# Performance work log

Hardware: AMD Instinct MI355X
Metric: run time of the kernel (lower is better)

Reference implementation:

```python
import jax, jax.numpy as jnp
import numpy as np

H = W = 512
K = 16          # max instance id (ids 1..K; 0 = background)
N_SIGMA = 1
FG_W = 1.0
W_INST, W_VAR, W_SEED = 1.0, 10.0, 1.0


def _xym(h, w, dtype):
    # torch: linspace(0,1,512) grids, sliced to [:, :h, :w]
    x = jnp.linspace(0.0, 1.0, 512)[:w]
    y = jnp.linspace(0.0, 1.0, 512)[:h]
    xm = jnp.broadcast_to(x[None, :], (h, w))
    ym = jnp.broadcast_to(y[:, None], (h, w))
    return jnp.stack([xm, ym], 0).astype(dtype)  # [2,h,w]


def _lovasz_hinge(logits, labels):
    # logits, labels: flat [P]; labels in {0,1} float
    signs = 2.0 * labels - 1.0
    errors = 1.0 - logits * signs
    perm = jnp.argsort(-errors)           # descending sort
    errors_sorted = errors[perm]
    gt_sorted = labels[perm]
    gts = gt_sorted.sum()
    inter = gts - jnp.cumsum(gt_sorted)
    union = gts + jnp.cumsum(1.0 - gt_sorted)
    jac = 1.0 - inter / union
    grad = jnp.concatenate([jac[:1], jac[1:] - jac[:-1]])
    # lovasz grad is computed from .data (detached) in the torch impl
    return jnp.dot(jax.nn.relu(errors_sorted), jax.lax.stop_gradient(grad))


def _per_instance(mask, spatial_emb, sigma, seed, xym):
    # mask: [H,W] float {0,1}; spatial_emb: [2,H,W]; sigma: [n_sigma,H,W]; seed: [H,W]
    cnt = mask.sum()
    safe = jnp.maximum(cnt, 1.0)
    center = jnp.sum(xym * mask, (1, 2)) / safe                        # [2] (to_center=True)
    s = jnp.sum(sigma * mask, (1, 2)) / safe                           # [n_sigma]
    var = jnp.sum((sigma - jax.lax.stop_gradient(s)[:, None, None]) ** 2 * mask) / (N_SIGMA * safe)
    s_exp = jnp.exp(s * 10.0)
    dist = jnp.exp(-jnp.sum((spatial_emb - center[:, None, None]) ** 2 * s_exp[:, None, None], 0))  # [H,W]
    inst = _lovasz_hinge(dist.ravel() * 2.0 - 1.0, mask.ravel())
    seed_l = FG_W * jnp.sum((seed - jax.lax.stop_gradient(dist)) ** 2 * mask)
    present = cnt > 0
    z = jnp.zeros((), dist.dtype)
    return (jnp.where(present, var, z), jnp.where(present, inst, z),
            jnp.where(present, seed_l, z), present.astype(dist.dtype))


def _per_image(pred, inst, lab, xym):
    spatial_emb = jnp.tanh(pred[0:2]) + xym                            # [2,H,W]
    sigma = pred[2:2 + N_SIGMA]                                        # [n_sigma,H,W]
    seed = jax.nn.sigmoid(pred[2 + N_SIGMA])                           # [H,W]
    ids = jnp.arange(1, K + 1)
    masks = (inst[None] == ids[:, None, None]).astype(pred.dtype)      # [K,H,W]
    var, instl, seedl, pres = jax.vmap(
        _per_instance, in_axes=(0, None, None, None, None))(masks, spatial_emb, sigma, seed, xym)
    obj = pres.sum()
    safe_obj = jnp.maximum(obj, 1.0)
    bg = (lab == 0).astype(pred.dtype)
    seed_total = (jnp.sum(seed ** 2 * bg) + seedl.sum()) / float(H * W)
    return W_INST * instl.sum() / safe_obj + W_VAR * var.sum() / safe_obj + W_SEED * seed_total


def setup_inputs() -> dict:
    key = jax.random.key(0)
    k1, k2, k3 = jax.random.split(key, 3)
    prediction = jax.random.normal(k1, (8, 4, H, W), dtype=jnp.float32)
    instances = jax.random.randint(k2, (8, H, W), 0, K + 1, dtype=jnp.int32)
    labels = jax.random.randint(k3, (8, H, W), 0, 2, dtype=jnp.int32)
    return {"prediction": prediction, "instances": instances, "labels": labels}


def reference(prediction, instances, labels):
    xym = _xym(prediction.shape[2], prediction.shape[3], prediction.dtype)
    losses = jax.vmap(_per_image, in_axes=(0, 0, 0, None))(prediction, instances, labels, xym)
    return losses.mean() + prediction.sum() * 0.0
```

## Files before the change

kernel.cpp:

```cpp
#include <hip/hip_runtime.h>

#define HH 512
#define WW 512
#define NPIX (HH*WW)
#define KK 16
#define BB 8
#define NB 128
#define NBP 136
#define CHS 128
#define CHV 128

__device__ __forceinline__ float fast_rcp(float x){ return __builtin_amdgcn_rcpf(x); }
__device__ __forceinline__ float fast_tanh(float x){
  x = fminf(fmaxf(x, -15.f), 15.f);
  float t = __expf(2.f*x);
  return (t-1.f)*fast_rcp(t+1.f);
}
__device__ __forceinline__ float fast_sigmoid(float x){
  x = fminf(fmaxf(x, -30.f), 30.f);
  return fast_rcp(1.f+__expf(-x));
}

__device__ __forceinline__ float dpp_row_sum16(float v){
  v += __int_as_float(__builtin_amdgcn_update_dpp(0, __float_as_int(v), 0x111, 0xf, 0xf, true));
  v += __int_as_float(__builtin_amdgcn_update_dpp(0, __float_as_int(v), 0x112, 0xf, 0xf, true));
  v += __int_as_float(__builtin_amdgcn_update_dpp(0, __float_as_int(v), 0x114, 0xf, 0xf, true));
  v += __int_as_float(__builtin_amdgcn_update_dpp(0, __float_as_int(v), 0x118, 0xf, 0xf, true));
  return v;
}

__global__ void __launch_bounds__(256) k_sums(
    const float* __restrict__ pred, const int* __restrict__ inst,
    const int* __restrict__ lab, float* __restrict__ partial_s ,
    float* __restrict__ partial_b ) {
  const int bid = blockIdx.x;
  const int b  = bid & 7;
  const int ch = bid >> 3;
  const int tid = threadIdx.x;
  const int wave = tid >> 6, lane = tid & 63;
  __shared__ float lred[KK][16][5];
  __shared__ float lbg[4];
  const float inv = 1.f/511.f;
  const float* ps = pred + (size_t)b*4*NPIX + 2*NPIX;
  const float* pd = ps + NPIX;
  const int*   ib = inst + (size_t)b*NPIX;
  const int*   lb = lab  + (size_t)b*NPIX;
  const int p = ch*2048 + tid*8;
  int4   iv0 = *(const int4*)(ib + p),     iv1 = *(const int4*)(ib + p + 4);
  int4   lv0 = *(const int4*)(lb + p),     lv1 = *(const int4*)(lb + p + 4);
  float4 sv0 = *(const float4*)(ps + p),   sv1 = *(const float4*)(ps + p + 4);
  float4 dv0 = *(const float4*)(pd + p),   dv1 = *(const float4*)(pd + p + 4);
  const float ym  = (float)(p >> 9) * inv;
  const float xm0 = (float)(p & (WW-1)) * inv;
  int   ida[8] = {iv0.x, iv0.y, iv0.z, iv0.w, iv1.x, iv1.y, iv1.z, iv1.w};
  int   laa[8] = {lv0.x, lv0.y, lv0.z, lv0.w, lv1.x, lv1.y, lv1.z, lv1.w};
  float sga[8] = {sv0.x, sv0.y, sv0.z, sv0.w, sv1.x, sv1.y, sv1.z, sv1.w};
  float sda[8] = {dv0.x, dv0.y, dv0.z, dv0.w, dv1.x, dv1.y, dv1.z, dv1.w};
  float xja[8], sg2[8];
  #pragma unroll
  for (int j = 0; j < 8; ++j) {
    xja[j] = xm0 + (float)j*inv;
    sg2[j] = sga[j]*sga[j];
  }

  float sbg = 0.f;
  #pragma unroll
  for (int j = 0; j < 8; ++j)
    if (laa[j] == 0) { float sd = fast_sigmoid(sda[j]); sbg += sd*sd; }
  #pragma unroll
  for (int off = 32; off; off >>= 1) sbg += __shfl_down(sbg, off);
  if (lane == 0) lbg[wave] = sbg;

  #pragma unroll
  for (int k = 0; k < KK; ++k) {
    float c = 0.f, sx = 0.f, ss = 0.f, sq = 0.f;
    #pragma unroll
    for (int j = 0; j < 8; ++j) {
      float m = (ida[j] == k+1) ? 1.f : 0.f;
      c  += m;
      sx = fmaf(m, xja[j], sx);
      ss = fmaf(m, sga[j], ss);
      sq = fmaf(m, sg2[j], sq);
    }
    c  = dpp_row_sum16(c);
    sx = dpp_row_sum16(sx);
    ss = dpp_row_sum16(ss);
    sq = dpp_row_sum16(sq);
    if ((lane & 15) == 15) {
      int g = wave*4 + (lane >> 4);
      lred[k][g][0] = c;  lred[k][g][1] = sx; lred[k][g][2] = c*ym;
      lred[k][g][3] = ss; lred[k][g][4] = sq;
    }
  }
  __syncthreads();
  if (tid < KK) {
    #pragma unroll
    for (int comp = 0; comp < 5; ++comp) {
      float a = 0.f;
      #pragma unroll
      for (int g = 0; g < 16; ++g) a += lred[tid][g][comp];
      partial_s[((size_t)b*80 + tid*5 + comp)*CHS + ch] = a;
    }
  }
  if (tid == 64) partial_b[bid] = lbg[0] + lbg[1] + lbg[2] + lbg[3];
}

__global__ void __launch_bounds__(128) k_reduce(
    const float* __restrict__ partial_s, float* __restrict__ der) {
  const int seg = blockIdx.x;
  const int b = seg >> 4, k = seg & 15;
  const int tid = threadIdx.x;
  const int w = tid >> 6, l = tid & 63;
  __shared__ float red5[5][2];
  #pragma unroll
  for (int comp = 0; comp < 5; ++comp) {
    const float* row = partial_s + ((size_t)b*80 + k*5 + comp)*CHS;
    float a = row[tid];
    #pragma unroll
    for (int off = 32; off; off >>= 1) a += __shfl_down(a, off);
    if (l == 0) red5[comp][w] = a;
  }
  __syncthreads();
  if (tid == 0) {
    float cnt = red5[0][0]+red5[0][1];
    float sx  = red5[1][0]+red5[1][1];
    float sy  = red5[2][0]+red5[2][1];
    float ss  = red5[3][0]+red5[3][1];
    float sq  = red5[4][0]+red5[4][1];
    float safe = fmaxf(cnt, 1.f);
    float rs = fast_rcp(safe);
    float sb = ss*rs;
    float* dd = der + seg*8;
    dd[0] = sx*rs; dd[1] = sy*rs;
    dd[2] = __expf(10.f*sb);
    dd[3] = (cnt > 0.f) ? 1.f : 0.f;
    dd[4] = sb;
    dd[5] = cnt;
    dd[6] = sq - cnt*sb*sb;
  }
}

__global__ void __launch_bounds__(256, 4) k_hist(
    const float* __restrict__ pred, const int* __restrict__ inst,
    const float* __restrict__ der, unsigned int* __restrict__ hist,
    float* __restrict__ partial_v ) {
  const int bid = blockIdx.x;
  const int b  = bid & 7;
  const int ch = bid >> 3;
  const int tid = threadIdx.x;
  const int g = tid >> 4, l4 = tid & 15;
  __shared__ unsigned int lh[KK][NBP];
  __shared__ float sder[KK][4];
  __shared__ float lsl[4];
  if (tid < KK) {
    const float* dd = der + (b*KK + tid)*8;
    sder[tid][0] = dd[0]; sder[tid][1] = dd[1]; sder[tid][2] = dd[2];
  }
  for (int i = tid; i < KK*NBP; i += 256) ((unsigned int*)lh)[i] = 0u;
  __syncthreads();
  const float L2E = 1.4426950408889634f;
  float seaL[KK], AL[KK], BL[KK], CL[KK];
  #pragma unroll
  for (int k = 0; k < KK; ++k) {
    float cx = sder[k][0], cy = sder[k][1], se = sder[k][2];
    float seL = se * L2E;
    seaL[k] = -seL;
    AL[k] = 2.f*cx*seL;
    BL[k] = 2.f*cy*seL;
    CL[k] = -(cx*cx + cy*cy)*seL;
  }
  const float inv = 1.f/511.f;
  const float* pbx = pred + (size_t)b*4*NPIX;
  const float* pby = pbx + NPIX;
  const float* pbd = pbx + 3*NPIX;
  const int*   ib  = inst + (size_t)b*NPIX;
  const int base = ch*2048 + g*128;
  float sloss = 0.f;
  #pragma unroll
  for (int it = 0; it < 2; ++it) {
    const int p = base + it*64 + l4*4;
    float4 px = *(const float4*)(pbx + p);
    float4 py = *(const float4*)(pby + p);
    int4   iv = *(const int4*)(ib + p);
    float4 dv = *(const float4*)(pbd + p);
    const float ym  = (float)(p >> 9) * inv;
    const float xm0 = (float)(p & (WW-1)) * inv;
    float pxa[4] = {px.x, px.y, px.z, px.w};
    float pya[4] = {py.x, py.y, py.z, py.w};
    int   ida[4] = {iv.x, iv.y, iv.z, iv.w};
    float sda[4] = {dv.x, dv.y, dv.z, dv.w};
    #pragma unroll
    for (int j = 0; j < 4; ++j) {
      float sex = fast_tanh(pxa[j]) + xm0 + (float)j*inv;
      float sey = fast_tanh(pya[j]) + ym;
      float s2 = fmaf(sex, sex, sey*sey);
      int id = ida[j];
      float down = 0.f;
      #pragma unroll
      for (int k = 0; k < KK; ++k) {
        float t2 = fmaf(seaL[k], s2, fmaf(AL[k], sex, fmaf(BL[k], sey, CL[k])));
        float d = __builtin_amdgcn_exp2f(t2);
        bool fg = (id == k+1);
        float dN = d * (float)NB;
        float uN = fg ? ((float)NB - dN) : dN;
        int bkt = (int)uN;
        bkt = bkt < (NB-1) ? bkt : (NB-1);
        atomicAdd(&lh[k][bkt], fg ? 0x10001u : 1u);
        down = fg ? d : down;
      }
      if (id >= 1) {
        float dsee = fast_sigmoid(sda[j]) - down;
        sloss = fmaf(dsee, dsee, sloss);
      }
    }
  }
  __syncthreads();
  #pragma unroll
  for (int k = 0; k < KK; ++k) {
    unsigned int* gh = hist + ((size_t)(b*KK + k)*CHV + ch)*NB;
    if (tid < NB) gh[tid] = lh[k][tid];
  }
  #pragma unroll
  for (int off = 32; off; off >>= 1) sloss += __shfl_down(sloss, off);
  if ((tid & 63) == 0) lsl[tid >> 6] = sloss;
  __syncthreads();
  if (tid == 0) partial_v[bid] = lsl[0] + lsl[1] + lsl[2] + lsl[3];
}

__global__ void __launch_bounds__(256) k_lovasz(
    const unsigned int* __restrict__ hist, const float* __restrict__ der,
    const float* __restrict__ partial_v, const float* __restrict__ partial_b,
    float* __restrict__ instl, unsigned int* __restrict__ done,
    float* __restrict__ out) {
  const int seg = blockIdx.x;
  const int tid = threadIdx.x;
  __shared__ float nbL[NB], fbL[NB];
  __shared__ unsigned int sOld;
  const float gts = der[seg*8 + 5];
  const unsigned int* h = hist + (size_t)seg*CHV*NB;
  if (tid < NB) {
    unsigned int nlo = 0, nhi = 0;
    #pragma unroll 8
    for (int c = 0; c < CHV; ++c) {
      unsigned int v = h[(size_t)c*NB + tid];
      nlo += v & 0xffffu; nhi += v >> 16;
    }
    nbL[tid] = (float)nlo; fbL[tid] = (float)nhi;
  }
  __syncthreads();
  if (tid < 64) {
    const int lane = tid;
    float lsum = 0.f;
    if (gts > 0.f) {
      float carryN = 0.f, carryF = 0.f;
      #pragma unroll
      for (int it = 0; it < NB/64; ++it) {
        int bkt = NB - 1 - (it*64 + lane);
        float nb = nbL[bkt], fb = fbL[bkt];
        float sn = nb, sf = fb;
        #pragma unroll
        for (int off = 1; off < 64; off <<= 1) {
          float tn = __shfl_up(sn, off);
          float tf = __shfl_up(sf, off);
          if (lane >= off) { sn += tn; sf += tf; }
        }
        float Nb = carryN + sn - nb;
        float Fb = carryF + sf - fb;
        if (nb > 0.f) {
          float e  = ((float)bkt + 0.5f) * (2.0f/(float)NB);
          float j0 = 1.f - (gts - Fb) / (gts + Nb - Fb);
          float N1 = Nb + nb, F1 = Fb + fb;
          float j1 = 1.f - (gts - F1) / (gts + N1 - F1);
          lsum += e * (j1 - j0);
        }
        carryN += __shfl(sn, 63);
        carryF += __shfl(sf, 63);
      }
      #pragma unroll
      for (int off = 32; off; off >>= 1) lsum += __shfl_down(lsum, off);
    }
    if (lane == 0) {
      instl[seg] = lsum;
      __threadfence();
      sOld = atomicAdd(done, 1u);
    }
  }
  __syncthreads();
  if ((sOld & 127u) != 127u) return;
  __threadfence();
  __shared__ float vtmp[256], btmp[256];
  {
    const int b8 = tid >> 5, j = tid & 31;
    float a = 0.f, c = 0.f;
    #pragma unroll
    for (int i = 0; i < 4; ++i) {
      a += partial_v[(size_t)(j + 32*i)*8 + b8];
      c += partial_b[(size_t)(j + 32*i)*8 + b8];
    }
    vtmp[tid] = a; btmp[tid] = c;
  }
  __syncthreads();
  float myv = 0.f;
  if (tid < BB) {
    int b = tid;
    float svl = 0.f, sbg = 0.f;
    #pragma unroll
    for (int j = 0; j < 32; ++j) { svl += vtmp[b*32 + j]; sbg += btmp[b*32 + j]; }
    float obj = 0.f, il = 0.f, vr = 0.f;
    for (int k = 0; k < KK; ++k) {
      int s2 = b*KK + k;
      float cnt = der[s2*8 + 5];
      if (cnt > 0.f) {
        obj += 1.f;
        il  += instl[s2];
        vr  += der[s2*8 + 6] / cnt;
      }
    }
    float so = fmaxf(obj, 1.f);
    myv = il/so + 10.f*vr/so + (sbg + svl)/(float)NPIX;
  }
  #pragma unroll
  for (int off = 4; off; off >>= 1) myv += __shfl_down(myv, off);
  if (tid == 0) out[0] = myv * (1.f/(float)BB);
}

extern "C" void kernel_launch(void* const* d_in, const int* in_sizes, int n_in,
                              void* d_out, int out_size, void* d_ws, size_t ws_size,
                              hipStream_t stream) {
  const float* pred = (const float*)d_in[0];
  const int*   inst = (const int*)d_in[1];
  const int*   lab  = (const int*)d_in[2];
  float* out = (float*)d_out;

  float* der         = (float*)d_ws;
  float* instl       = (float*)((char*)d_ws + 4160);
  unsigned int* done = (unsigned int*)((char*)d_ws + 4736);
  float* partial_b   = (float*)((char*)d_ws + 8192);
  float* partial_v   = (float*)((char*)d_ws + 16384);
  float* partial_s   = (float*)((char*)d_ws + 24576);
  unsigned int* hist = (unsigned int*)((char*)d_ws + 679936);

  k_sums  <<<BB*CHS, 256, 0, stream>>>(pred, inst, lab, partial_s, partial_b);
  k_reduce<<<BB*KK, 128, 0, stream>>>(partial_s, der);
  k_hist  <<<BB*CHV, 256, 0, stream>>>(pred, inst, der, hist, partial_v);
  k_lovasz<<<BB*KK, 256, 0, stream>>>(hist, der, partial_v, partial_b,
                                      instl, done, out);
}
```

Baseline: 53.46 us.

## Fold per-instance reduction into histogram and lovasz kernels, drop k_reduce launch

Removes the separate k_reduce kernel. Each k_hist block now re-reduces the 128 channel partials for its image's 16 instances itself, and k_lovasz reduces the count, sigma sum and square-sum it needs. The NB scaling is folded into the exponent constant as +7 in log2 space, which saves a multiply per instance-pixel. The seed-loss distance is recomputed only for the pixel's own instance, so a select per instance is no longer needed. In exchange, every k_hist block does redundant serial loads of partial sums (64 threads each summing 128 values), which adds latency at the start of each block.

```diff
diff --git a/kernel.cpp b/kernel.cpp
--- a/kernel.cpp
+++ b/kernel.cpp
@@ -105,44 +105,9 @@
   if (tid == 64) partial_b[bid] = lbg[0] + lbg[1] + lbg[2] + lbg[3];
 }
 
-__global__ void __launch_bounds__(128) k_reduce(
-    const float* __restrict__ partial_s, float* __restrict__ der) {
-  const int seg = blockIdx.x;
-  const int b = seg >> 4, k = seg & 15;
-  const int tid = threadIdx.x;
-  const int w = tid >> 6, l = tid & 63;
-  __shared__ float red5[5][2];
-  #pragma unroll
-  for (int comp = 0; comp < 5; ++comp) {
-    const float* row = partial_s + ((size_t)b*80 + k*5 + comp)*CHS;
-    float a = row[tid];
-    #pragma unroll
-    for (int off = 32; off; off >>= 1) a += __shfl_down(a, off);
-    if (l == 0) red5[comp][w] = a;
-  }
-  __syncthreads();
-  if (tid == 0) {
-    float cnt = red5[0][0]+red5[0][1];
-    float sx  = red5[1][0]+red5[1][1];
-    float sy  = red5[2][0]+red5[2][1];
-    float ss  = red5[3][0]+red5[3][1];
-    float sq  = red5[4][0]+red5[4][1];
-    float safe = fmaxf(cnt, 1.f);
-    float rs = fast_rcp(safe);
-    float sb = ss*rs;
-    float* dd = der + seg*8;
-    dd[0] = sx*rs; dd[1] = sy*rs;
-    dd[2] = __expf(10.f*sb);
-    dd[3] = (cnt > 0.f) ? 1.f : 0.f;
-    dd[4] = sb;
-    dd[5] = cnt;
-    dd[6] = sq - cnt*sb*sb;
-  }
-}
-
 __global__ void __launch_bounds__(256, 4) k_hist(
     const float* __restrict__ pred, const int* __restrict__ inst,
-    const float* __restrict__ der, unsigned int* __restrict__ hist,
+    const float* __restrict__ partial_s, unsigned int* __restrict__ hist,
     float* __restrict__ partial_v ) {
   const int bid = blockIdx.x;
   const int b  = bid & 7;
@@ -150,16 +115,29 @@
   const int tid = threadIdx.x;
   const int g = tid >> 4, l4 = tid & 15;
   __shared__ unsigned int lh[KK][NBP];
-  __shared__ float sder[KK][4];
+  __shared__ float sred[KK][4];
+  __shared__ float sder[KK][3];
   __shared__ float lsl[4];
+  if (tid < 64) {
+    int k = tid >> 2, comp = tid & 3;
+    const float* row = partial_s + ((size_t)b*80 + k*5 + comp)*CHS;
+    float a = 0.f;
+    #pragma unroll 8
+    for (int c = 0; c < CHS; ++c) a += row[c];
+    sred[k][comp] = a;
+  } else {
+    for (int i = tid - 64; i < KK*NBP; i += 192) ((unsigned int*)lh)[i] = 0u;
+  }
+  __syncthreads();
   if (tid < KK) {
-    const float* dd = der + (b*KK + tid)*8;
-    sder[tid][0] = dd[0]; sder[tid][1] = dd[1]; sder[tid][2] = dd[2];
-  }
-  for (int i = tid; i < KK*NBP; i += 256) ((unsigned int*)lh)[i] = 0u;
+    float rs = fast_rcp(fmaxf(sred[tid][0], 1.f));
+    sder[tid][0] = sred[tid][1]*rs;
+    sder[tid][1] = sred[tid][2]*rs;
+    sder[tid][2] = __expf(10.f*sred[tid][3]*rs);
+  }
   __syncthreads();
   const float L2E = 1.4426950408889634f;
-  float seaL[KK], AL[KK], BL[KK], CL[KK];
+  float seaL[KK], AL[KK], BL[KK], CL7[KK];
   #pragma unroll
   for (int k = 0; k < KK; ++k) {
     float cx = sder[k][0], cy = sder[k][1], se = sder[k][2];
@@ -167,7 +145,7 @@
     seaL[k] = -seL;
     AL[k] = 2.f*cx*seL;
     BL[k] = 2.f*cy*seL;
-    CL[k] = -(cx*cx + cy*cy)*seL;
+    CL7[k] = 7.f - (cx*cx + cy*cy)*seL;
   }
   const float inv = 1.f/511.f;
   const float* pbx = pred + (size_t)b*4*NPIX;
@@ -195,21 +173,21 @@
       float sey = fast_tanh(pya[j]) + ym;
       float s2 = fmaf(sex, sex, sey*sey);
       int id = ida[j];
-      float down = 0.f;
       #pragma unroll
       for (int k = 0; k < KK; ++k) {
-        float t2 = fmaf(seaL[k], s2, fmaf(AL[k], sex, fmaf(BL[k], sey, CL[k])));
-        float d = __builtin_amdgcn_exp2f(t2);
+        float t2 = fmaf(seaL[k], s2, fmaf(AL[k], sex, fmaf(BL[k], sey, CL7[k])));
+        float dN = __builtin_amdgcn_exp2f(t2);
         bool fg = (id == k+1);
-        float dN = d * (float)NB;
         float uN = fg ? ((float)NB - dN) : dN;
         int bkt = (int)uN;
         bkt = bkt < (NB-1) ? bkt : (NB-1);
         atomicAdd(&lh[k][bkt], fg ? 0x10001u : 1u);
-        down = fg ? d : down;
       }
       if (id >= 1) {
-        float dsee = fast_sigmoid(sda[j]) - down;
+        float cx = sder[id-1][0], cy = sder[id-1][1], se = sder[id-1][2];
+        float dx = sex - cx, dy = sey - cy;
+        float dwn = __builtin_amdgcn_exp2f(-se*L2E*fmaf(dx,dx,dy*dy));
+        float dsee = fast_sigmoid(sda[j]) - dwn;
         sloss = fmaf(dsee, dsee, sloss);
       }
     }
@@ -228,15 +206,16 @@
 }
 
 __global__ void __launch_bounds__(256) k_lovasz(
-    const unsigned int* __restrict__ hist, const float* __restrict__ der,
+    const unsigned int* __restrict__ hist, const float* __restrict__ partial_s,
     const float* __restrict__ partial_v, const float* __restrict__ partial_b,
-    float* __restrict__ instl, unsigned int* __restrict__ done,
-    float* __restrict__ out) {
+    float* __restrict__ instl, float* __restrict__ der2,
+    unsigned int* __restrict__ done, float* __restrict__ out) {
   const int seg = blockIdx.x;
+  const int b = seg >> 4, k = seg & 15;
   const int tid = threadIdx.x;
   __shared__ float nbL[NB], fbL[NB];
+  __shared__ float s3[3];
   __shared__ unsigned int sOld;
-  const float gts = der[seg*8 + 5];
   const unsigned int* h = hist + (size_t)seg*CHV*NB;
   if (tid < NB) {
     unsigned int nlo = 0, nhi = 0;
@@ -246,8 +225,16 @@
       nlo += v & 0xffffu; nhi += v >> 16;
     }
     nbL[tid] = (float)nlo; fbL[tid] = (float)nhi;
-  }
-  __syncthreads();
+  } else if (tid >= 128 && tid < 131) {
+    int comp = (tid == 128) ? 0 : (tid == 129) ? 3 : 4;
+    const float* row = partial_s + ((size_t)b*80 + k*5 + comp)*CHS;
+    float a = 0.f;
+    #pragma unroll 8
+    for (int c = 0; c < CHS; ++c) a += row[c];
+    s3[tid - 128] = a;
+  }
+  __syncthreads();
+  const float gts = s3[0];
   if (tid < 64) {
     const int lane = tid;
     float lsum = 0.f;
@@ -280,7 +267,11 @@
       for (int off = 32; off; off >>= 1) lsum += __shfl_down(lsum, off);
     }
     if (lane == 0) {
+      float cnt = gts;
+      float sb = s3[1] * fast_rcp(fmaxf(cnt, 1.f));
       instl[seg] = lsum;
+      der2[seg*2 + 0] = cnt;
+      der2[seg*2 + 1] = s3[2] - cnt*sb*sb;
       __threadfence();
       sOld = atomicAdd(done, 1u);
     }
@@ -302,18 +293,18 @@
   __syncthreads();
   float myv = 0.f;
   if (tid < BB) {
-    int b = tid;
+    int bb = tid;
     float svl = 0.f, sbg = 0.f;
     #pragma unroll
-    for (int j = 0; j < 32; ++j) { svl += vtmp[b*32 + j]; sbg += btmp[b*32 + j]; }
+    for (int j = 0; j < 32; ++j) { svl += vtmp[bb*32 + j]; sbg += btmp[bb*32 + j]; }
     float obj = 0.f, il = 0.f, vr = 0.f;
-    for (int k = 0; k < KK; ++k) {
-      int s2 = b*KK + k;
-      float cnt = der[s2*8 + 5];
+    for (int kk = 0; kk < KK; ++kk) {
+      int s2 = bb*KK + kk;
+      float cnt = der2[s2*2 + 0];
       if (cnt > 0.f) {
         obj += 1.f;
         il  += instl[s2];
-        vr  += der[s2*8 + 6] / cnt;
+        vr  += der2[s2*2 + 1] / cnt;
       }
     }
     float so = fmaxf(obj, 1.f);
@@ -332,17 +323,16 @@
   const int*   lab  = (const int*)d_in[2];
   float* out = (float*)d_out;
 
-  float* der         = (float*)d_ws;
-  float* instl       = (float*)((char*)d_ws + 4160);
-  unsigned int* done = (unsigned int*)((char*)d_ws + 4736);
+  float* instl       = (float*)d_ws;
+  float* der2        = (float*)((char*)d_ws + 1024);
+  unsigned int* done = (unsigned int*)((char*)d_ws + 2048);
   float* partial_b   = (float*)((char*)d_ws + 8192);
   float* partial_v   = (float*)((char*)d_ws + 16384);
   float* partial_s   = (float*)((char*)d_ws + 24576);
   unsigned int* hist = (unsigned int*)((char*)d_ws + 679936);
 
   k_sums  <<<BB*CHS, 256, 0, stream>>>(pred, inst, lab, partial_s, partial_b);
-  k_reduce<<<BB*KK, 128, 0, stream>>>(partial_s, der);
-  k_hist  <<<BB*CHV, 256, 0, stream>>>(pred, inst, der, hist, partial_v);
-  k_lovasz<<<BB*KK, 256, 0, stream>>>(hist, der, partial_v, partial_b,
-                                      instl, done, out);
-}
+  k_hist  <<<BB*CHV, 256, 0, stream>>>(pred, inst, partial_s, hist, partial_v);
+  k_lovasz<<<BB*KK, 256, 0, stream>>>(hist, partial_s, partial_v, partial_b,
+                                      instl, der2, done, out);
+}
```

Result: faster. 51.73 us (-3.2%).
